# Kernel optimization log

Hardware: AMD Instinct MI355X
Metric: run time of the kernel (lower is better)

## Reference

```python
import jax, jax.numpy as jnp
import numpy as np

N_NODES = 50000
N_EDGES = 400000
IN_DIM, HID_DIM, OUT_DIM = 512, 512, 128


def sage_conv(x, src, dst, W_l, b_l, W_r, n_nodes):
    # PyG SAGEConv (mean aggr): out = lin_l(mean_{j in N(i)} x_j) + lin_r(x_i)
    msgs = x[src]                                             # [E, d_in]
    agg = jax.ops.segment_sum(msgs, dst, num_segments=n_nodes)
    deg = jax.ops.segment_sum(jnp.ones((src.shape[0],), x.dtype), dst,
                              num_segments=n_nodes)
    mean = agg / jnp.maximum(deg, 1.0)[:, None]
    return mean @ W_l + b_l + x @ W_r


def setup_inputs() -> dict:
    key = jax.random.key(0)
    ks = jax.random.split(key, 9)
    x = jax.random.normal(ks[0], (N_NODES, IN_DIM), dtype=jnp.float32)
    edge_index = jax.random.randint(ks[1], (2, N_EDGES), 0, N_NODES, dtype=jnp.int32)

    def glorot(k, d_in, d_out):
        s = (6.0 / (d_in + d_out)) ** 0.5
        return jax.random.uniform(k, (d_in, d_out), jnp.float32, -s, s)

    return {
        "x": x,
        "edge_index": edge_index,
        "W1_l": glorot(ks[2], IN_DIM, HID_DIM),
        "b1": jnp.zeros((HID_DIM,), jnp.float32),
        "W1_r": glorot(ks[3], IN_DIM, HID_DIM),
        "W2_l": glorot(ks[4], HID_DIM, HID_DIM),
        "b2": jnp.zeros((HID_DIM,), jnp.float32),
        "W2_r": glorot(ks[5], HID_DIM, HID_DIM),
        "W3_l": glorot(ks[6], HID_DIM, OUT_DIM),
        "b3": jnp.zeros((OUT_DIM,), jnp.float32),
        "W3_r": glorot(ks[7], HID_DIM, OUT_DIM),
    }


def reference(x, edge_index, W1_l, b1, W1_r, W2_l, b2, W2_r, W3_l, b3, W3_r):
    src, dst = edge_index[0], edge_index[1]
    n = x.shape[0]
    h = sage_conv(x, src, dst, W1_l, b1, W1_r, n)
    h = jax.nn.relu(h)  # dropout is identity in eval mode
    h = sage_conv(h, src, dst, W2_l, b2, W2_r, n)
    h = jax.nn.relu(h)
    h = sage_conv(h, src, dst, W3_l, b3, W3_r, n)
    return jax.nn.log_softmax(h, axis=-1)
```

## Files before the change

kernel.cpp:

```cpp
#include <hip/hip_runtime.h>
#include <hip/hip_bf16.h>


#define N_NODES 50000
#define N_EDGES 400000

typedef unsigned short u16;
typedef unsigned int u32;
typedef __attribute__((ext_vector_type(8))) short short8;
typedef __attribute__((ext_vector_type(4))) float floatx4;

#define ASYNC16(g, l)                                                      \
    __builtin_amdgcn_global_load_lds(                                      \
        (const __attribute__((address_space(1))) void*)(g),                \
        (__attribute__((address_space(3))) void*)(l), 16, 0, 0)

__device__ __forceinline__ u16 f32_to_bf16(float f) {
    u32 u = __float_as_uint(f);
    u32 r = 0x7FFFu + ((u >> 16) & 1u);
    return (u16)((u + r) >> 16);
}
__device__ __forceinline__ float bf16_to_f32(u32 lo16) {
    return __uint_as_float(lo16 << 16);
}

__global__ __launch_bounds__(256) void zero4_kernel(float4* __restrict__ p, int n4) {
    int i = blockIdx.x * 256 + threadIdx.x;
    if (i < n4) p[i] = make_float4(0.f, 0.f, 0.f, 0.f);
}

__global__ __launch_bounds__(256) void hist_kernel(const int* __restrict__ dst,
                                                   int* __restrict__ deg, int E) {
    int e = blockIdx.x * 256 + threadIdx.x;
    if (e < E) atomicAdd(&deg[dst[e]], 1);
}

__global__ __launch_bounds__(256) void scan_reduce(const int* __restrict__ v,
                                                   int* __restrict__ bsums, int n) {
    __shared__ int sh[256];
    int i = blockIdx.x * 256 + threadIdx.x;
    sh[threadIdx.x] = (i < n) ? v[i] : 0;
    __syncthreads();
    for (int off = 128; off > 0; off >>= 1) {
        if (threadIdx.x < off) sh[threadIdx.x] += sh[threadIdx.x + off];
        __syncthreads();
    }
    if (threadIdx.x == 0) bsums[blockIdx.x] = sh[0];
}

__global__ __launch_bounds__(256) void scan_sums(int* __restrict__ bsums, int nb) {
    __shared__ int sh[256];
    int t = threadIdx.x;
    int val = (t < nb) ? bsums[t] : 0;
    sh[t] = val;
    __syncthreads();
    for (int off = 1; off < 256; off <<= 1) {
        int v = (t >= off) ? sh[t - off] : 0;
        __syncthreads();
        sh[t] += v;
        __syncthreads();
    }
    if (t < nb) bsums[t] = sh[t] - val;
}

__global__ __launch_bounds__(256) void scan_final(int* __restrict__ v,
                                                  const int* __restrict__ bsums, int n) {
    __shared__ int sh[256];
    int t = threadIdx.x;
    int i = blockIdx.x * 256 + t;
    int val = (i < n) ? v[i] : 0;
    sh[t] = val;
    __syncthreads();
    for (int off = 1; off < 256; off <<= 1) {
        int x = (t >= off) ? sh[t - off] : 0;
        __syncthreads();
        sh[t] += x;
        __syncthreads();
    }
    int excl = sh[t] - val + bsums[blockIdx.x];
    if (i < n) v[i] = excl;
    if (i == n - 1) v[n] = excl + val;
}

__global__ __launch_bounds__(256) void fill_kernel(const int* __restrict__ src,
                                                   const int* __restrict__ dst,
                                                   const int* __restrict__ row_start,
                                                   int* __restrict__ cursor,
                                                   int* __restrict__ csr_src, int E) {
    int e = blockIdx.x * 256 + threadIdx.x;
    if (e < E) {
        int d = dst[e];
        int pos = row_start[d] + atomicAdd(&cursor[d], 1);
        csr_src[pos] = src[e];
    }
}

__global__ __launch_bounds__(256) void convert_bf16(const float* __restrict__ in,
                                                    u16* __restrict__ out, int n8) {
    int i = blockIdx.x * 256 + threadIdx.x;
    if (i >= n8) return;
    const float4* p = (const float4*)in + (size_t)i * 2;
    float4 v0 = p[0], v1 = p[1];
    uint4 o;
    o.x = (u32)f32_to_bf16(v0.x) | ((u32)f32_to_bf16(v0.y) << 16);
    o.y = (u32)f32_to_bf16(v0.z) | ((u32)f32_to_bf16(v0.w) << 16);
    o.z = (u32)f32_to_bf16(v1.x) | ((u32)f32_to_bf16(v1.y) << 16);
    o.w = (u32)f32_to_bf16(v1.z) | ((u32)f32_to_bf16(v1.w) << 16);
    ((uint4*)out)[i] = o;
}

__global__ __launch_bounds__(256) void transpose_w(const float* __restrict__ W,
                                                   u16* __restrict__ WT,
                                                   int K, int N) {
    __shared__ float t[32][33];
    int n0 = blockIdx.x * 32, k0 = blockIdx.y * 32;
    int c = threadIdx.x & 31, r0 = threadIdx.x >> 5;
    for (int r = r0; r < 32; r += 8)
        t[r][c] = W[(size_t)(k0 + r) * N + n0 + c];
    __syncthreads();
    for (int r = r0; r < 32; r += 8)
        WT[(size_t)(n0 + r) * K + k0 + c] = f32_to_bf16(t[c][r]);
}

__global__ __launch_bounds__(256) void gemm_bf16(
    const u16* __restrict__ A, const u16* __restrict__ BT,
    u16* __restrict__ Cl, u16* __restrict__ Cr,
    int M, int split, int nStrips, int nCols) {
    __shared__ u16 As[2][4096];
    __shared__ u16 Bs[2][4096];

    const int grp = 8 * nCols;
    int b = blockIdx.x;
    int strip = (b / grp) * 8 + (b & 7);
    int colt = (b % grp) >> 3;
    if (strip >= nStrips) return;
    const int row0 = strip * 128, col0 = colt * 128;

    const int t = threadIdx.x;
    const int w = t >> 6, lane = t & 63;
    const int wm = (w >> 1) * 64, wn = (w & 1) * 64;
    const int l15 = lane & 15, kq = lane >> 4;
    const int swz = (l15 >> 1) & 3;

    floatx4 acc[4][4];
#pragma unroll
    for (int i = 0; i < 4; ++i)
#pragma unroll
        for (int j = 0; j < 4; ++j) acc[i][j] = floatx4{0.f, 0.f, 0.f, 0.f};

    const int sr = t >> 2;
    const int sc = t & 3;
    const int swzS = (sr >> 1) & 3;
    const size_t aA0 = (size_t)min(row0 + sr, M - 1) * 512 + (sc ^ swzS) * 8;
    const size_t aA1 = (size_t)min(row0 + 64 + sr, M - 1) * 512 + (sc ^ swzS) * 8;
    const size_t aB0 = (size_t)(col0 + sr) * 512 + (sc ^ swzS) * 8;
    const size_t aB1 = (size_t)(col0 + 64 + sr) * 512 + (sc ^ swzS) * 8;
    const int d0 = w * 512;
    const int d1 = 2048 + w * 512;

    auto stage = [&](int it, int buf) {
        const int eff = it * 32;
        ASYNC16(A + aA0 + eff, &As[buf][d0]);
        ASYNC16(A + aA1 + eff, &As[buf][d1]);
        ASYNC16(BT + aB0 + eff, &Bs[buf][d0]);
        ASYNC16(BT + aB1 + eff, &Bs[buf][d1]);
    };

    stage(0, 0);
    __syncthreads();
    for (int it = 0; it < 16; ++it) {
        const int buf = it & 1;
        if (it + 1 < 16) stage(it + 1, buf ^ 1);

        const int kc = (kq ^ swz) * 8;
        short8 a[4], bfr[4];
#pragma unroll
        for (int mt = 0; mt < 4; ++mt)
            a[mt] = *(const short8*)&As[buf][(wm + mt * 16 + l15) * 32 + kc];
#pragma unroll
        for (int nt = 0; nt < 4; ++nt)
            bfr[nt] = *(const short8*)&Bs[buf][(wn + nt * 16 + l15) * 32 + kc];
#pragma unroll
        for (int mt = 0; mt < 4; ++mt)
#pragma unroll
            for (int nt = 0; nt < 4; ++nt)
                acc[mt][nt] = __builtin_amdgcn_mfma_f32_16x16x32_bf16(
                    bfr[nt], a[mt], acc[mt][nt], 0, 0, 0);
        __syncthreads();
    }

    u16* __restrict__ Cbase = (col0 < split) ? Cl : Cr;
    const int cadj = (col0 < split) ? col0 : (col0 - split);
#pragma unroll
    for (int mt = 0; mt < 4; ++mt) {
        int row = row0 + wm + mt * 16 + l15;
        if (row >= M) continue;
#pragma unroll
        for (int nt = 0; nt < 4; ++nt) {
            int c0 = cadj + wn + nt * 16 + kq * 4;
            uint2 o;
            o.x = (u32)f32_to_bf16(acc[mt][nt][0]) |
                  ((u32)f32_to_bf16(acc[mt][nt][1]) << 16);
            o.y = (u32)f32_to_bf16(acc[mt][nt][2]) |
                  ((u32)f32_to_bf16(acc[mt][nt][3]) << 16);
            *(uint2*)(Cbase + (size_t)row * split + c0) = o;
        }
    }
}

__global__ __launch_bounds__(256) void gather_add_relu512(
    const u16* __restrict__ Yl, const u16* __restrict__ Yr,
    const float* __restrict__ bias,
    const int* __restrict__ row_start, const int* __restrict__ csr_src,
    u16* __restrict__ h, int M) {
    int node = (blockIdx.x * 256 + threadIdx.x) >> 6;
    int lane = threadIdx.x & 63;
    if (node >= M) return;
    int beg = row_start[node], end = row_start[node + 1];
    float a[8] = {0.f, 0.f, 0.f, 0.f, 0.f, 0.f, 0.f, 0.f};
    for (int c = beg; c < end; c += 64) {
        int nb = min(64, end - c);
        int eid = (lane < nb) ? csr_src[c + lane] : 0;
        for (int i = 0; i < nb; ++i) {
            int s = __shfl(eid, i);
            uint4 v = ((const uint4*)(Yl + (size_t)s * 512))[lane];
            a[0] += bf16_to_f32(v.x & 0xffffu); a[1] += bf16_to_f32(v.x >> 16);
            a[2] += bf16_to_f32(v.y & 0xffffu); a[3] += bf16_to_f32(v.y >> 16);
            a[4] += bf16_to_f32(v.z & 0xffffu); a[5] += bf16_to_f32(v.z >> 16);
            a[6] += bf16_to_f32(v.w & 0xffffu); a[7] += bf16_to_f32(v.w >> 16);
        }
    }
    float inv = 1.0f / fmaxf((float)(end - beg), 1.0f);
    uint4 yr = ((const uint4*)(Yr + (size_t)node * 512))[lane];
    float4 b0 = ((const float4*)bias)[lane * 2];
    float4 b1 = ((const float4*)bias)[lane * 2 + 1];
    float v0 = fmaxf(a[0] * inv + bf16_to_f32(yr.x & 0xffffu) + b0.x, 0.f);
    float v1 = fmaxf(a[1] * inv + bf16_to_f32(yr.x >> 16)     + b0.y, 0.f);
    float v2 = fmaxf(a[2] * inv + bf16_to_f32(yr.y & 0xffffu) + b0.z, 0.f);
    float v3 = fmaxf(a[3] * inv + bf16_to_f32(yr.y >> 16)     + b0.w, 0.f);
    float v4 = fmaxf(a[4] * inv + bf16_to_f32(yr.z & 0xffffu) + b1.x, 0.f);
    float v5 = fmaxf(a[5] * inv + bf16_to_f32(yr.z >> 16)     + b1.y, 0.f);
    float v6 = fmaxf(a[6] * inv + bf16_to_f32(yr.w & 0xffffu) + b1.z, 0.f);
    float v7 = fmaxf(a[7] * inv + bf16_to_f32(yr.w >> 16)     + b1.w, 0.f);
    uint4 o;
    o.x = (u32)f32_to_bf16(v0) | ((u32)f32_to_bf16(v1) << 16);
    o.y = (u32)f32_to_bf16(v2) | ((u32)f32_to_bf16(v3) << 16);
    o.z = (u32)f32_to_bf16(v4) | ((u32)f32_to_bf16(v5) << 16);
    o.w = (u32)f32_to_bf16(v6) | ((u32)f32_to_bf16(v7) << 16);
    ((uint4*)(h + (size_t)node * 512))[lane] = o;
}

__global__ __launch_bounds__(256) void gather_add_lsm128(
    const u16* __restrict__ Yl, const u16* __restrict__ Yr,
    const float* __restrict__ bias,
    const int* __restrict__ row_start, const int* __restrict__ csr_src,
    float* __restrict__ out, int M) {
    int node = blockIdx.x * 16 + (threadIdx.x >> 4);
    int lane = threadIdx.x & 63;
    int li = lane & 15;
    int gbase = lane & 48;
    if (node >= M) return;
    int beg = row_start[node], end = row_start[node + 1];
    float a[8] = {0.f, 0.f, 0.f, 0.f, 0.f, 0.f, 0.f, 0.f};
    for (int c = beg; c < end; c += 16) {
        int nb = min(16, end - c);
        int eid = (li < nb) ? csr_src[c + li] : 0;
        for (int i = 0; i < nb; ++i) {
            int s = __shfl(eid, gbase + i);
            uint4 v = ((const uint4*)(Yl + (size_t)s * 128))[li];
            a[0] += bf16_to_f32(v.x & 0xffffu); a[1] += bf16_to_f32(v.x >> 16);
            a[2] += bf16_to_f32(v.y & 0xffffu); a[3] += bf16_to_f32(v.y >> 16);
            a[4] += bf16_to_f32(v.z & 0xffffu); a[5] += bf16_to_f32(v.z >> 16);
            a[6] += bf16_to_f32(v.w & 0xffffu); a[7] += bf16_to_f32(v.w >> 16);
        }
    }
    float inv = 1.0f / fmaxf((float)(end - beg), 1.0f);
    uint4 yr = ((const uint4*)(Yr + (size_t)node * 128))[li];
    float4 b0 = ((const float4*)bias)[li * 2];
    float4 b1 = ((const float4*)bias)[li * 2 + 1];
    float v[8];
    v[0] = a[0] * inv + bf16_to_f32(yr.x & 0xffffu) + b0.x;
    v[1] = a[1] * inv + bf16_to_f32(yr.x >> 16)     + b0.y;
    v[2] = a[2] * inv + bf16_to_f32(yr.y & 0xffffu) + b0.z;
    v[3] = a[3] * inv + bf16_to_f32(yr.y >> 16)     + b0.w;
    v[4] = a[4] * inv + bf16_to_f32(yr.z & 0xffffu) + b1.x;
    v[5] = a[5] * inv + bf16_to_f32(yr.z >> 16)     + b1.y;
    v[6] = a[6] * inv + bf16_to_f32(yr.w & 0xffffu) + b1.z;
    v[7] = a[7] * inv + bf16_to_f32(yr.w >> 16)     + b1.w;
    float m = v[0];
#pragma unroll
    for (int j = 1; j < 8; ++j) m = fmaxf(m, v[j]);
#pragma unroll
    for (int off = 1; off < 16; off <<= 1) m = fmaxf(m, __shfl_xor(m, off));
    float s = 0.f;
#pragma unroll
    for (int j = 0; j < 8; ++j) s += expf(v[j] - m);
#pragma unroll
    for (int off = 1; off < 16; off <<= 1) s += __shfl_xor(s, off);
    float ls = m + logf(s);
    float* p = out + (size_t)node * 128 + li * 8;
    *(float4*)p       = make_float4(v[0] - ls, v[1] - ls, v[2] - ls, v[3] - ls);
    *(float4*)(p + 4) = make_float4(v[4] - ls, v[5] - ls, v[6] - ls, v[7] - ls);
}

extern "C" void kernel_launch(void* const* d_in, const int* in_sizes, int n_in,
                              void* d_out, int out_size, void* d_ws, size_t ws_size,
                              hipStream_t stream) {
    const float* x    = (const float*)d_in[0];
    const int*   ei   = (const int*)d_in[1];
    const float* W1_l = (const float*)d_in[2];
    const float* b1   = (const float*)d_in[3];
    const float* W1_r = (const float*)d_in[4];
    const float* W2_l = (const float*)d_in[5];
    const float* b2   = (const float*)d_in[6];
    const float* W2_r = (const float*)d_in[7];
    const float* W3_l = (const float*)d_in[8];
    const float* b3   = (const float*)d_in[9];
    const float* W3_r = (const float*)d_in[10];
    float* out = (float*)d_out;

    const int* src = ei;
    const int* dst = ei + N_EDGES;

    char* base = (char*)d_ws;
    int* row_start = (int*)(base);
    int* cursor    = (int*)(base + 200208);
    int* bsums     = (int*)(base + 400416);
    int* csr_src   = (int*)(base + 402464);
    u16* xb  = (u16*)(base + 2002464);
    u16* h1b = (u16*)(base + 53202464);
    u16* h2b = (u16*)(base + 104402464);
    u16* Yl  = (u16*)(base + 155602464);
    u16* Yr  = (u16*)(base + 206802464);
    u16* w1T = (u16*)(base + 258002464);
    u16* w2T = (u16*)(base + 259051040);
    u16* w3T = (u16*)(base + 260099616);

    const int E = N_EDGES, M = N_NODES;
    const int nblk = (M + 255) / 256;

    zero4_kernel<<<(25154 + 255) / 256, 256, 0, stream>>>((float4*)d_ws, 25154);
    hist_kernel<<<(E + 255) / 256, 256, 0, stream>>>(dst, row_start, E);
    scan_reduce<<<nblk, 256, 0, stream>>>(row_start, bsums, M);
    scan_sums<<<1, 256, 0, stream>>>(bsums, nblk);
    scan_final<<<nblk, 256, 0, stream>>>(row_start, bsums, M);
    fill_kernel<<<(E + 255) / 256, 256, 0, stream>>>(src, dst, row_start, cursor,
                                                     csr_src, E);

    convert_bf16<<<(3200000 + 255) / 256, 256, 0, stream>>>(x, xb, 3200000);
    transpose_w<<<dim3(16, 16), 256, 0, stream>>>(W1_l, w1T, 512, 512);
    transpose_w<<<dim3(16, 16), 256, 0, stream>>>(W1_r, w1T + 512 * 512, 512, 512);
    transpose_w<<<dim3(16, 16), 256, 0, stream>>>(W2_l, w2T, 512, 512);
    transpose_w<<<dim3(16, 16), 256, 0, stream>>>(W2_r, w2T + 512 * 512, 512, 512);
    transpose_w<<<dim3(4, 16), 256, 0, stream>>>(W3_l, w3T, 512, 128);
    transpose_w<<<dim3(4, 16), 256, 0, stream>>>(W3_r, w3T + 128 * 512, 512, 128);

    const int nStrips = (M + 127) / 128;
    const int grid8 = ((nStrips + 7) / 8) * 64;
    const int grid2 = ((nStrips + 7) / 8) * 16;
    const int gblocks = (M * 64 + 255) / 256;
    const int g16blocks = (M + 15) / 16;

    gemm_bf16<<<grid8, 256, 0, stream>>>(xb, w1T, Yl, Yr, M, 512, nStrips, 8);
    gather_add_relu512<<<gblocks, 256, 0, stream>>>(Yl, Yr, b1, row_start,
                                                    csr_src, h1b, M);
    gemm_bf16<<<grid8, 256, 0, stream>>>(h1b, w2T, Yl, Yr, M, 512, nStrips, 8);
    gather_add_relu512<<<gblocks, 256, 0, stream>>>(Yl, Yr, b2, row_start,
                                                    csr_src, h2b, M);
    gemm_bf16<<<grid2, 256, 0, stream>>>(h2b, w3T, Yl, Yr, M, 128, nStrips, 2);
    gather_add_lsm128<<<g16blocks, 256, 0, stream>>>(Yl, Yr, b3, row_start,
                                                     csr_src, out, M);
}
```

Before: 656.8 us.

## Make each GEMM block loop over several column tiles with a continuous pipeline

Each GEMM workgroup now processes nCT consecutive 128-column tiles for its row strip instead of one. It runs a single double-buffered k-loop across all tiles and stores and resets the accumulators at each tile boundary. This cuts block count (4x for the 512-wide layers, 2x for the last) and keeps prefetching going across tiles, amortizing launch and prologue cost. In exchange there are fewer blocks to spread over the CUs, which may hurt occupancy and load balance, and the A tile is reloaded from global/L2 for every column tile.

After: 762.7 us. +16.1%, slower.

```diff
diff --git a/kernel.cpp b/kernel.cpp
--- a/kernel.cpp
+++ b/kernel.cpp
@@ -125,16 +125,17 @@
 __global__ __launch_bounds__(256) void gemm_bf16(
     const u16* __restrict__ A, const u16* __restrict__ BT,
     u16* __restrict__ Cl, u16* __restrict__ Cr,
-    int M, int split, int nStrips, int nCols) {
+    int M, int split, int nStrips, int nGrp, int nCT) {
     __shared__ u16 As[2][4096];
     __shared__ u16 Bs[2][4096];
 
-    const int grp = 8 * nCols;
+    const int grp = 8 * nGrp;
     int b = blockIdx.x;
     int strip = (b / grp) * 8 + (b & 7);
-    int colt = (b % grp) >> 3;
+    int ctg = (b % grp) >> 3;
     if (strip >= nStrips) return;
-    const int row0 = strip * 128, col0 = colt * 128;
+    const int row0 = strip * 128;
+    const int col0base = ctg * nCT * 128;
 
     const int t = threadIdx.x;
     const int w = t >> 6, lane = t & 63;
@@ -153,24 +154,52 @@
     const int swzS = (sr >> 1) & 3;
     const size_t aA0 = (size_t)min(row0 + sr, M - 1) * 512 + (sc ^ swzS) * 8;
     const size_t aA1 = (size_t)min(row0 + 64 + sr, M - 1) * 512 + (sc ^ swzS) * 8;
-    const size_t aB0 = (size_t)(col0 + sr) * 512 + (sc ^ swzS) * 8;
-    const size_t aB1 = (size_t)(col0 + 64 + sr) * 512 + (sc ^ swzS) * 8;
+    const size_t aB0 = (size_t)(col0base + sr) * 512 + (sc ^ swzS) * 8;
+    const size_t aB1 = (size_t)(col0base + 64 + sr) * 512 + (sc ^ swzS) * 8;
     const int d0 = w * 512;
     const int d1 = 2048 + w * 512;
 
-    auto stage = [&](int it, int buf) {
-        const int eff = it * 32;
-        ASYNC16(A + aA0 + eff, &As[buf][d0]);
-        ASYNC16(A + aA1 + eff, &As[buf][d1]);
-        ASYNC16(BT + aB0 + eff, &Bs[buf][d0]);
-        ASYNC16(BT + aB1 + eff, &Bs[buf][d1]);
+    auto stage = [&](int tt, int buf) {
+        const int it = tt & 15, ct = tt >> 4;
+        const size_t effA = (size_t)it * 32;
+        const size_t effB = (size_t)ct * 65536 + effA;
+        ASYNC16(A + aA0 + effA, &As[buf][d0]);
+        ASYNC16(A + aA1 + effA, &As[buf][d1]);
+        ASYNC16(BT + aB0 + effB, &Bs[buf][d0]);
+        ASYNC16(BT + aB1 + effB, &Bs[buf][d1]);
     };
 
+    auto storeCT = [&](int ct) {
+        const int col0 = col0base + ct * 128;
+        u16* __restrict__ Cbase = (col0 < split) ? Cl : Cr;
+        const int cadj = (col0 < split) ? col0 : (col0 - split);
+#pragma unroll
+        for (int mt = 0; mt < 4; ++mt) {
+            int row = row0 + wm + mt * 16 + l15;
+            if (row >= M) continue;
+#pragma unroll
+            for (int nt = 0; nt < 4; ++nt) {
+                int c0 = cadj + wn + nt * 16 + kq * 4;
+                uint2 o;
+                o.x = (u32)f32_to_bf16(acc[mt][nt][0]) |
+                      ((u32)f32_to_bf16(acc[mt][nt][1]) << 16);
+                o.y = (u32)f32_to_bf16(acc[mt][nt][2]) |
+                      ((u32)f32_to_bf16(acc[mt][nt][3]) << 16);
+                *(uint2*)(Cbase + (size_t)row * split + c0) = o;
+            }
+        }
+#pragma unroll
+        for (int i = 0; i < 4; ++i)
+#pragma unroll
+            for (int j = 0; j < 4; ++j) acc[i][j] = floatx4{0.f, 0.f, 0.f, 0.f};
+    };
+
+    const int nT = nCT * 16;
     stage(0, 0);
     __syncthreads();
-    for (int it = 0; it < 16; ++it) {
-        const int buf = it & 1;
-        if (it + 1 < 16) stage(it + 1, buf ^ 1);
+    for (int tt = 0; tt < nT; ++tt) {
+        const int buf = tt & 1;
+        if (tt + 1 < nT) stage(tt + 1, buf ^ 1);
 
         const int kc = (kq ^ swz) * 8;
         short8 a[4], bfr[4];
@@ -186,25 +215,10 @@
             for (int nt = 0; nt < 4; ++nt)
                 acc[mt][nt] = __builtin_amdgcn_mfma_f32_16x16x32_bf16(
                     bfr[nt], a[mt], acc[mt][nt], 0, 0, 0);
-        __syncthreads();
-    }
-
-    u16* __restrict__ Cbase = (col0 < split) ? Cl : Cr;
-    const int cadj = (col0 < split) ? col0 : (col0 - split);
-#pragma unroll
-    for (int mt = 0; mt < 4; ++mt) {
-        int row = row0 + wm + mt * 16 + l15;
-        if (row >= M) continue;
-#pragma unroll
-        for (int nt = 0; nt < 4; ++nt) {
-            int c0 = cadj + wn + nt * 16 + kq * 4;
-            uint2 o;
-            o.x = (u32)f32_to_bf16(acc[mt][nt][0]) |
-                  ((u32)f32_to_bf16(acc[mt][nt][1]) << 16);
-            o.y = (u32)f32_to_bf16(acc[mt][nt][2]) |
-                  ((u32)f32_to_bf16(acc[mt][nt][3]) << 16);
-            *(uint2*)(Cbase + (size_t)row * split + c0) = o;
-        }
+
+        if ((tt & 15) == 15) storeCT(tt >> 4);
+
+        if (tt + 1 < nT) __syncthreads();
     }
 }
 
@@ -356,18 +370,18 @@
     transpose_w<<<dim3(4, 16), 256, 0, stream>>>(W3_r, w3T + 128 * 512, 512, 128);
 
     const int nStrips = (M + 127) / 128;
-    const int grid8 = ((nStrips + 7) / 8) * 64;
-    const int grid2 = ((nStrips + 7) / 8) * 16;
+    const int grid12 = ((nStrips + 7) / 8) * 16;
+    const int grid3  = ((nStrips + 7) / 8) * 8;
     const int gblocks = (M * 64 + 255) / 256;
     const int g16blocks = (M + 15) / 16;
 
-    gemm_bf16<<<grid8, 256, 0, stream>>>(xb, w1T, Yl, Yr, M, 512, nStrips, 8);
+    gemm_bf16<<<grid12, 256, 0, stream>>>(xb, w1T, Yl, Yr, M, 512, nStrips, 2, 4);
     gather_add_relu512<<<gblocks, 256, 0, stream>>>(Yl, Yr, b1, row_start,
                                                     csr_src, h1b, M);
-    gemm_bf16<<<grid8, 256, 0, stream>>>(h1b, w2T, Yl, Yr, M, 512, nStrips, 8);
+    gemm_bf16<<<grid12, 256, 0, stream>>>(h1b, w2T, Yl, Yr, M, 512, nStrips, 2, 4);
     gather_add_relu512<<<gblocks, 256, 0, stream>>>(Yl, Yr, b2, row_start,
                                                     csr_src, h2b, M);
-    gemm_bf16<<<grid2, 256, 0, stream>>>(h2b, w3T, Yl, Yr, M, 128, nStrips, 2);
+    gemm_bf16<<<grid3, 256, 0, stream>>>(h2b, w3T, Yl, Yr, M, 128, nStrips, 1, 2);
     gather_add_lsm128<<<g16blocks, 256, 0, stream>>>(Yl, Yr, b3, row_start,
                                                      csr_src, out, M);
 }
```

## Switch GEMM to single-wave 64x64 tiles with waitcnt-based double buffering

Applied to the files above, without the earlier changes.

The bf16 GEMM moves from a 256-thread block computing a 128x128 tile to a 64-thread, single-wave block computing a 64x64 tile. The grid is resized to match. Because only one wave touches the LDS buffers, the __syncthreads barriers are replaced by explicit s_waitcnt vmcnt waits on the async global-to-LDS loads, plus a sched_barrier. This is meant to cut barrier stalls and give the scheduler more, smaller blocks, at the cost of lower data reuse per tile and more global/L2 traffic for A and B.

New measurement: 774.7 us. 1.18x slower.

```diff
diff --git a/kernel.cpp b/kernel.cpp
--- a/kernel.cpp
+++ b/kernel.cpp
@@ -122,23 +122,21 @@
         WT[(size_t)(n0 + r) * K + k0 + c] = f32_to_bf16(t[c][r]);
 }
 
-__global__ __launch_bounds__(256) void gemm_bf16(
+__global__ __launch_bounds__(64) void gemm_bf16(
     const u16* __restrict__ A, const u16* __restrict__ BT,
     u16* __restrict__ Cl, u16* __restrict__ Cr,
     int M, int split, int nStrips, int nCols) {
-    __shared__ u16 As[2][4096];
-    __shared__ u16 Bs[2][4096];
+    __shared__ u16 As[2][2048];
+    __shared__ u16 Bs[2][2048];
 
     const int grp = 8 * nCols;
     int b = blockIdx.x;
     int strip = (b / grp) * 8 + (b & 7);
     int colt = (b % grp) >> 3;
     if (strip >= nStrips) return;
-    const int row0 = strip * 128, col0 = colt * 128;
-
-    const int t = threadIdx.x;
-    const int w = t >> 6, lane = t & 63;
-    const int wm = (w >> 1) * 64, wn = (w & 1) * 64;
+    const int row0 = strip * 64, col0 = colt * 64;
+
+    const int lane = threadIdx.x;
     const int l15 = lane & 15, kq = lane >> 4;
     const int swz = (l15 >> 1) & 3;
 
@@ -148,56 +146,61 @@
 #pragma unroll
         for (int j = 0; j < 4; ++j) acc[i][j] = floatx4{0.f, 0.f, 0.f, 0.f};
 
-    const int sr = t >> 2;
-    const int sc = t & 3;
+    const int sr = lane >> 2;
+    const int sc = lane & 3;
     const int swzS = (sr >> 1) & 3;
-    const size_t aA0 = (size_t)min(row0 + sr, M - 1) * 512 + (sc ^ swzS) * 8;
-    const size_t aA1 = (size_t)min(row0 + 64 + sr, M - 1) * 512 + (sc ^ swzS) * 8;
-    const size_t aB0 = (size_t)(col0 + sr) * 512 + (sc ^ swzS) * 8;
-    const size_t aB1 = (size_t)(col0 + 64 + sr) * 512 + (sc ^ swzS) * 8;
-    const int d0 = w * 512;
-    const int d1 = 2048 + w * 512;
+    size_t aoff[4], boff[4];
+#pragma unroll
+    for (int g = 0; g < 4; ++g) {
+        aoff[g] = (size_t)min(row0 + g * 16 + sr, M - 1) * 512 + (sc ^ swzS) * 8;
+        boff[g] = (size_t)(col0 + g * 16 + sr) * 512 + (sc ^ swzS) * 8;
+    }
 
     auto stage = [&](int it, int buf) {
         const int eff = it * 32;
-        ASYNC16(A + aA0 + eff, &As[buf][d0]);
-        ASYNC16(A + aA1 + eff, &As[buf][d1]);
-        ASYNC16(BT + aB0 + eff, &Bs[buf][d0]);
-        ASYNC16(BT + aB1 + eff, &Bs[buf][d1]);
+#pragma unroll
+        for (int g = 0; g < 4; ++g) {
+            ASYNC16(A + aoff[g] + eff, &As[buf][g * 512]);
+            ASYNC16(BT + boff[g] + eff, &Bs[buf][g * 512]);
+        }
     };
 
     stage(0, 0);
-    __syncthreads();
     for (int it = 0; it < 16; ++it) {
         const int buf = it & 1;
-        if (it + 1 < 16) stage(it + 1, buf ^ 1);
+        if (it + 1 < 16) {
+            stage(it + 1, buf ^ 1);
+            asm volatile("s_waitcnt vmcnt(8)" ::: "memory");
+        } else {
+            asm volatile("s_waitcnt vmcnt(0)" ::: "memory");
+        }
+        __builtin_amdgcn_sched_barrier(0);
 
         const int kc = (kq ^ swz) * 8;
         short8 a[4], bfr[4];
 #pragma unroll
         for (int mt = 0; mt < 4; ++mt)
-            a[mt] = *(const short8*)&As[buf][(wm + mt * 16 + l15) * 32 + kc];
+            a[mt] = *(const short8*)&As[buf][(mt * 16 + l15) * 32 + kc];
 #pragma unroll
         for (int nt = 0; nt < 4; ++nt)
-            bfr[nt] = *(const short8*)&Bs[buf][(wn + nt * 16 + l15) * 32 + kc];
+            bfr[nt] = *(const short8*)&Bs[buf][(nt * 16 + l15) * 32 + kc];
 #pragma unroll
         for (int mt = 0; mt < 4; ++mt)
 #pragma unroll
             for (int nt = 0; nt < 4; ++nt)
                 acc[mt][nt] = __builtin_amdgcn_mfma_f32_16x16x32_bf16(
                     bfr[nt], a[mt], acc[mt][nt], 0, 0, 0);
-        __syncthreads();
     }
 
     u16* __restrict__ Cbase = (col0 < split) ? Cl : Cr;
     const int cadj = (col0 < split) ? col0 : (col0 - split);
 #pragma unroll
     for (int mt = 0; mt < 4; ++mt) {
-        int row = row0 + wm + mt * 16 + l15;
+        int row = row0 + mt * 16 + l15;
         if (row >= M) continue;
 #pragma unroll
         for (int nt = 0; nt < 4; ++nt) {
-            int c0 = cadj + wn + nt * 16 + kq * 4;
+            int c0 = cadj + nt * 16 + kq * 4;
             uint2 o;
             o.x = (u32)f32_to_bf16(acc[mt][nt][0]) |
                   ((u32)f32_to_bf16(acc[mt][nt][1]) << 16);
@@ -355,19 +358,19 @@
     transpose_w<<<dim3(4, 16), 256, 0, stream>>>(W3_l, w3T, 512, 128);
     transpose_w<<<dim3(4, 16), 256, 0, stream>>>(W3_r, w3T + 128 * 512, 512, 128);
 
-    const int nStrips = (M + 127) / 128;
-    const int grid8 = ((nStrips + 7) / 8) * 64;
-    const int grid2 = ((nStrips + 7) / 8) * 16;
+    const int nStrips = (M + 63) / 64;
+    const int grid12 = ((nStrips + 7) / 8) * 8 * 16;
+    const int grid3  = ((nStrips + 7) / 8) * 8 * 4;
     const int gblocks = (M * 64 + 255) / 256;
     const int g16blocks = (M + 15) / 16;
 
-    gemm_bf16<<<grid8, 256, 0, stream>>>(xb, w1T, Yl, Yr, M, 512, nStrips, 8);
+    gemm_bf16<<<grid12, 64, 0, stream>>>(xb, w1T, Yl, Yr, M, 512, nStrips, 16);
     gather_add_relu512<<<gblocks, 256, 0, stream>>>(Yl, Yr, b1, row_start,
                                                     csr_src, h1b, M);
-    gemm_bf16<<<grid8, 256, 0, stream>>>(h1b, w2T, Yl, Yr, M, 512, nStrips, 8);
+    gemm_bf16<<<grid12, 64, 0, stream>>>(h1b, w2T, Yl, Yr, M, 512, nStrips, 16);
     gather_add_relu512<<<gblocks, 256, 0, stream>>>(Yl, Yr, b2, row_start,
                                                     csr_src, h2b, M);
-    gemm_bf16<<<grid2, 256, 0, stream>>>(h2b, w3T, Yl, Yr, M, 128, nStrips, 2);
+    gemm_bf16<<<grid3, 64, 0, stream>>>(h2b, w3T, Yl, Yr, M, 128, nStrips, 4);
     gather_add_lsm128<<<g16blocks, 256, 0, stream>>>(Yl, Yr, b3, row_start,
                                                      csr_src, out, M);
 }
```

## Aggregate before transform and fuse both linears into one K=1024 GEMM

Applied to the files above, without the earlier changes.

Each layer now gathers the neighbour mean of the input features first, then runs one GEMM over the concatenated [x | mean] with stacked weights (K=1024), adding bias and ReLU in the GEMM epilogue. Before, a 2N-wide GEMM wrote separate Yl/Yr tensors, which the gather then read back. The new order removes that Yr round trip and the split output, and the final layer no longer needs the 128-wide gather. The trade-off is that the gather in layer 3 now reads 512-wide rows instead of 128-wide ones. The gather loop is also unrolled by four to keep more loads in flight.

New measurement: 727.7 us. 10.8% more time.

```diff
diff --git a/kernel.cpp b/kernel.cpp
--- a/kernel.cpp
+++ b/kernel.cpp
@@ -111,7 +111,7 @@
 
 __global__ __launch_bounds__(256) void transpose_w(const float* __restrict__ W,
                                                    u16* __restrict__ WT,
-                                                   int K, int N) {
+                                                   int K, int N, int kstride, int koff) {
     __shared__ float t[32][33];
     int n0 = blockIdx.x * 32, k0 = blockIdx.y * 32;
     int c = threadIdx.x & 31, r0 = threadIdx.x >> 5;
@@ -119,13 +119,13 @@
         t[r][c] = W[(size_t)(k0 + r) * N + n0 + c];
     __syncthreads();
     for (int r = r0; r < 32; r += 8)
-        WT[(size_t)(n0 + r) * K + k0 + c] = f32_to_bf16(t[c][r]);
-}
-
-__global__ __launch_bounds__(256) void gemm_bf16(
-    const u16* __restrict__ A, const u16* __restrict__ BT,
-    u16* __restrict__ Cl, u16* __restrict__ Cr,
-    int M, int split, int nStrips, int nCols) {
+        WT[(size_t)(n0 + r) * kstride + koff + k0 + c] = f32_to_bf16(t[c][r]);
+}
+
+__global__ __launch_bounds__(256) void gemm_bias(
+    const u16* __restrict__ A0, const u16* __restrict__ A1,
+    const u16* __restrict__ BT, const float* __restrict__ bias,
+    u16* __restrict__ C, int M, int N, int nStrips, int nCols, int relu) {
     __shared__ u16 As[2][4096];
     __shared__ u16 Bs[2][4096];
 
@@ -153,24 +153,26 @@
     const int swzS = (sr >> 1) & 3;
     const size_t aA0 = (size_t)min(row0 + sr, M - 1) * 512 + (sc ^ swzS) * 8;
     const size_t aA1 = (size_t)min(row0 + 64 + sr, M - 1) * 512 + (sc ^ swzS) * 8;
-    const size_t aB0 = (size_t)(col0 + sr) * 512 + (sc ^ swzS) * 8;
-    const size_t aB1 = (size_t)(col0 + 64 + sr) * 512 + (sc ^ swzS) * 8;
+    const size_t bB0 = (size_t)(col0 + sr) * 1024 + (sc ^ swzS) * 8;
+    const size_t bB1 = (size_t)(col0 + 64 + sr) * 1024 + (sc ^ swzS) * 8;
     const int d0 = w * 512;
     const int d1 = 2048 + w * 512;
 
     auto stage = [&](int it, int buf) {
-        const int eff = it * 32;
-        ASYNC16(A + aA0 + eff, &As[buf][d0]);
-        ASYNC16(A + aA1 + eff, &As[buf][d1]);
-        ASYNC16(BT + aB0 + eff, &Bs[buf][d0]);
-        ASYNC16(BT + aB1 + eff, &Bs[buf][d1]);
+        const u16* __restrict__ Asrc = (it < 16) ? A0 : A1;
+        const int effA = (it & 15) * 32;
+        const int effB = it * 32;
+        ASYNC16(Asrc + aA0 + effA, &As[buf][d0]);
+        ASYNC16(Asrc + aA1 + effA, &As[buf][d1]);
+        ASYNC16(BT + bB0 + effB, &Bs[buf][d0]);
+        ASYNC16(BT + bB1 + effB, &Bs[buf][d1]);
     };
 
     stage(0, 0);
     __syncthreads();
-    for (int it = 0; it < 16; ++it) {
+    for (int it = 0; it < 32; ++it) {
         const int buf = it & 1;
-        if (it + 1 < 16) stage(it + 1, buf ^ 1);
+        if (it + 1 < 32) stage(it + 1, buf ^ 1);
 
         const int kc = (kq ^ swz) * 8;
         short8 a[4], bfr[4];
@@ -189,30 +191,41 @@
         __syncthreads();
     }
 
-    u16* __restrict__ Cbase = (col0 < split) ? Cl : Cr;
-    const int cadj = (col0 < split) ? col0 : (col0 - split);
 #pragma unroll
     for (int mt = 0; mt < 4; ++mt) {
         int row = row0 + wm + mt * 16 + l15;
         if (row >= M) continue;
 #pragma unroll
         for (int nt = 0; nt < 4; ++nt) {
-            int c0 = cadj + wn + nt * 16 + kq * 4;
+            int c0 = col0 + wn + nt * 16 + kq * 4;
+            float4 bv = *(const float4*)(bias + c0);
+            float v0 = acc[mt][nt][0] + bv.x;
+            float v1 = acc[mt][nt][1] + bv.y;
+            float v2 = acc[mt][nt][2] + bv.z;
+            float v3 = acc[mt][nt][3] + bv.w;
+            if (relu) {
+                v0 = fmaxf(v0, 0.f); v1 = fmaxf(v1, 0.f);
+                v2 = fmaxf(v2, 0.f); v3 = fmaxf(v3, 0.f);
+            }
             uint2 o;
-            o.x = (u32)f32_to_bf16(acc[mt][nt][0]) |
-                  ((u32)f32_to_bf16(acc[mt][nt][1]) << 16);
-            o.y = (u32)f32_to_bf16(acc[mt][nt][2]) |
-                  ((u32)f32_to_bf16(acc[mt][nt][3]) << 16);
-            *(uint2*)(Cbase + (size_t)row * split + c0) = o;
+            o.x = (u32)f32_to_bf16(v0) | ((u32)f32_to_bf16(v1) << 16);
+            o.y = (u32)f32_to_bf16(v2) | ((u32)f32_to_bf16(v3) << 16);
+            *(uint2*)(C + (size_t)row * N + c0) = o;
         }
     }
 }
 
-__global__ __launch_bounds__(256) void gather_add_relu512(
-    const u16* __restrict__ Yl, const u16* __restrict__ Yr,
-    const float* __restrict__ bias,
+__device__ __forceinline__ void acc8(float* a, uint4 v) {
+    a[0] += bf16_to_f32(v.x & 0xffffu); a[1] += bf16_to_f32(v.x >> 16);
+    a[2] += bf16_to_f32(v.y & 0xffffu); a[3] += bf16_to_f32(v.y >> 16);
+    a[4] += bf16_to_f32(v.z & 0xffffu); a[5] += bf16_to_f32(v.z >> 16);
+    a[6] += bf16_to_f32(v.w & 0xffffu); a[7] += bf16_to_f32(v.w >> 16);
+}
+
+__global__ __launch_bounds__(256) void gather_mean512(
+    const u16* __restrict__ S,
     const int* __restrict__ row_start, const int* __restrict__ csr_src,
-    u16* __restrict__ h, int M) {
+    u16* __restrict__ mx, int M) {
     int node = (blockIdx.x * 256 + threadIdx.x) >> 6;
     int lane = threadIdx.x & 63;
     if (node >= M) return;
@@ -221,72 +234,44 @@
     for (int c = beg; c < end; c += 64) {
         int nb = min(64, end - c);
         int eid = (lane < nb) ? csr_src[c + lane] : 0;
-        for (int i = 0; i < nb; ++i) {
+        int i = 0;
+        for (; i + 4 <= nb; i += 4) {
+            int s0 = __shfl(eid, i);
+            int s1 = __shfl(eid, i + 1);
+            int s2 = __shfl(eid, i + 2);
+            int s3 = __shfl(eid, i + 3);
+            uint4 v0 = ((const uint4*)(S + (size_t)s0 * 512))[lane];
+            uint4 v1 = ((const uint4*)(S + (size_t)s1 * 512))[lane];
+            uint4 v2 = ((const uint4*)(S + (size_t)s2 * 512))[lane];
+            uint4 v3 = ((const uint4*)(S + (size_t)s3 * 512))[lane];
+            acc8(a, v0); acc8(a, v1); acc8(a, v2); acc8(a, v3);
+        }
+        for (; i < nb; ++i) {
             int s = __shfl(eid, i);
-            uint4 v = ((const uint4*)(Yl + (size_t)s * 512))[lane];
-            a[0] += bf16_to_f32(v.x & 0xffffu); a[1] += bf16_to_f32(v.x >> 16);
-            a[2] += bf16_to_f32(v.y & 0xffffu); a[3] += bf16_to_f32(v.y >> 16);
-            a[4] += bf16_to_f32(v.z & 0xffffu); a[5] += bf16_to_f32(v.z >> 16);
-            a[6] += bf16_to_f32(v.w & 0xffffu); a[7] += bf16_to_f32(v.w >> 16);
+            uint4 v = ((const uint4*)(S + (size_t)s * 512))[lane];
+            acc8(a, v);
         }
     }
     float inv = 1.0f / fmaxf((float)(end - beg), 1.0f);
-    uint4 yr = ((const uint4*)(Yr + (size_t)node * 512))[lane];
-    float4 b0 = ((const float4*)bias)[lane * 2];
-    float4 b1 = ((const float4*)bias)[lane * 2 + 1];
-    float v0 = fmaxf(a[0] * inv + bf16_to_f32(yr.x & 0xffffu) + b0.x, 0.f);
-    float v1 = fmaxf(a[1] * inv + bf16_to_f32(yr.x >> 16)     + b0.y, 0.f);
-    float v2 = fmaxf(a[2] * inv + bf16_to_f32(yr.y & 0xffffu) + b0.z, 0.f);
-    float v3 = fmaxf(a[3] * inv + bf16_to_f32(yr.y >> 16)     + b0.w, 0.f);
-    float v4 = fmaxf(a[4] * inv + bf16_to_f32(yr.z & 0xffffu) + b1.x, 0.f);
-    float v5 = fmaxf(a[5] * inv + bf16_to_f32(yr.z >> 16)     + b1.y, 0.f);
-    float v6 = fmaxf(a[6] * inv + bf16_to_f32(yr.w & 0xffffu) + b1.z, 0.f);
-    float v7 = fmaxf(a[7] * inv + bf16_to_f32(yr.w >> 16)     + b1.w, 0.f);
     uint4 o;
-    o.x = (u32)f32_to_bf16(v0) | ((u32)f32_to_bf16(v1) << 16);
-    o.y = (u32)f32_to_bf16(v2) | ((u32)f32_to_bf16(v3) << 16);
-    o.z = (u32)f32_to_bf16(v4) | ((u32)f32_to_bf16(v5) << 16);
-    o.w = (u32)f32_to_bf16(v6) | ((u32)f32_to_bf16(v7) << 16);
-    ((uint4*)(h + (size_t)node * 512))[lane] = o;
-}
-
-__global__ __launch_bounds__(256) void gather_add_lsm128(
-    const u16* __restrict__ Yl, const u16* __restrict__ Yr,
-    const float* __restrict__ bias,
-    const int* __restrict__ row_start, const int* __restrict__ csr_src,
-    float* __restrict__ out, int M) {
+    o.x = (u32)f32_to_bf16(a[0] * inv) | ((u32)f32_to_bf16(a[1] * inv) << 16);
+    o.y = (u32)f32_to_bf16(a[2] * inv) | ((u32)f32_to_bf16(a[3] * inv) << 16);
+    o.z = (u32)f32_to_bf16(a[4] * inv) | ((u32)f32_to_bf16(a[5] * inv) << 16);
+    o.w = (u32)f32_to_bf16(a[6] * inv) | ((u32)f32_to_bf16(a[7] * inv) << 16);
+    ((uint4*)(mx + (size_t)node * 512))[lane] = o;
+}
+
+__global__ __launch_bounds__(256) void lsm_dense128(
+    const u16* __restrict__ Y, float* __restrict__ out, int M) {
     int node = blockIdx.x * 16 + (threadIdx.x >> 4);
-    int lane = threadIdx.x & 63;
-    int li = lane & 15;
-    int gbase = lane & 48;
+    int li = threadIdx.x & 15;
     if (node >= M) return;
-    int beg = row_start[node], end = row_start[node + 1];
-    float a[8] = {0.f, 0.f, 0.f, 0.f, 0.f, 0.f, 0.f, 0.f};
-    for (int c = beg; c < end; c += 16) {
-        int nb = min(16, end - c);
-        int eid = (li < nb) ? csr_src[c + li] : 0;
-        for (int i = 0; i < nb; ++i) {
-            int s = __shfl(eid, gbase + i);
-            uint4 v = ((const uint4*)(Yl + (size_t)s * 128))[li];
-            a[0] += bf16_to_f32(v.x & 0xffffu); a[1] += bf16_to_f32(v.x >> 16);
-            a[2] += bf16_to_f32(v.y & 0xffffu); a[3] += bf16_to_f32(v.y >> 16);
-            a[4] += bf16_to_f32(v.z & 0xffffu); a[5] += bf16_to_f32(v.z >> 16);
-            a[6] += bf16_to_f32(v.w & 0xffffu); a[7] += bf16_to_f32(v.w >> 16);
-        }
-    }
-    float inv = 1.0f / fmaxf((float)(end - beg), 1.0f);
-    uint4 yr = ((const uint4*)(Yr + (size_t)node * 128))[li];
-    float4 b0 = ((const float4*)bias)[li * 2];
-    float4 b1 = ((const float4*)bias)[li * 2 + 1];
+    uint4 yv = ((const uint4*)(Y + (size_t)node * 128))[li];
     float v[8];
-    v[0] = a[0] * inv + bf16_to_f32(yr.x & 0xffffu) + b0.x;
-    v[1] = a[1] * inv + bf16_to_f32(yr.x >> 16)     + b0.y;
-    v[2] = a[2] * inv + bf16_to_f32(yr.y & 0xffffu) + b0.z;
-    v[3] = a[3] * inv + bf16_to_f32(yr.y >> 16)     + b0.w;
-    v[4] = a[4] * inv + bf16_to_f32(yr.z & 0xffffu) + b1.x;
-    v[5] = a[5] * inv + bf16_to_f32(yr.z >> 16)     + b1.y;
-    v[6] = a[6] * inv + bf16_to_f32(yr.w & 0xffffu) + b1.z;
-    v[7] = a[7] * inv + bf16_to_f32(yr.w >> 16)     + b1.w;
+    v[0] = bf16_to_f32(yv.x & 0xffffu); v[1] = bf16_to_f32(yv.x >> 16);
+    v[2] = bf16_to_f32(yv.y & 0xffffu); v[3] = bf16_to_f32(yv.y >> 16);
+    v[4] = bf16_to_f32(yv.z & 0xffffu); v[5] = bf16_to_f32(yv.z >> 16);
+    v[6] = bf16_to_f32(yv.w & 0xffffu); v[7] = bf16_to_f32(yv.w >> 16);
     float m = v[0];
 #pragma unroll
     for (int j = 1; j < 8; ++j) m = fmaxf(m, v[j]);
@@ -330,11 +315,11 @@
     u16* xb  = (u16*)(base + 2002464);
     u16* h1b = (u16*)(base + 53202464);
     u16* h2b = (u16*)(base + 104402464);
-    u16* Yl  = (u16*)(base + 155602464);
-    u16* Yr  = (u16*)(base + 206802464);
-    u16* w1T = (u16*)(base + 258002464);
-    u16* w2T = (u16*)(base + 259051040);
-    u16* w3T = (u16*)(base + 260099616);
+    u16* mx  = (u16*)(base + 155602464);
+    u16* y3  = (u16*)(base + 206802464);
+    u16* w1T = (u16*)(base + 219602464);
+    u16* w2T = (u16*)(base + 220651040);
+    u16* w3T = (u16*)(base + 221699616);
 
     const int E = N_EDGES, M = N_NODES;
     const int nblk = (M + 255) / 256;
@@ -348,26 +333,27 @@
                                                      csr_src, E);
 
     convert_bf16<<<(3200000 + 255) / 256, 256, 0, stream>>>(x, xb, 3200000);
-    transpose_w<<<dim3(16, 16), 256, 0, stream>>>(W1_l, w1T, 512, 512);
-    transpose_w<<<dim3(16, 16), 256, 0, stream>>>(W1_r, w1T + 512 * 512, 512, 512);
-    transpose_w<<<dim3(16, 16), 256, 0, stream>>>(W2_l, w2T, 512, 512);
-    transpose_w<<<dim3(16, 16), 256, 0, stream>>>(W2_r, w2T + 512 * 512, 512, 512);
-    transpose_w<<<dim3(4, 16), 256, 0, stream>>>(W3_l, w3T, 512, 128);
-    transpose_w<<<dim3(4, 16), 256, 0, stream>>>(W3_r, w3T + 128 * 512, 512, 128);
+    transpose_w<<<dim3(16, 16), 256, 0, stream>>>(W1_r, w1T, 512, 512, 1024, 0);
+    transpose_w<<<dim3(16, 16), 256, 0, stream>>>(W1_l, w1T, 512, 512, 1024, 512);
+    transpose_w<<<dim3(16, 16), 256, 0, stream>>>(W2_r, w2T, 512, 512, 1024, 0);
+    transpose_w<<<dim3(16, 16), 256, 0, stream>>>(W2_l, w2T, 512, 512, 1024, 512);
+    transpose_w<<<dim3(4, 16), 256, 0, stream>>>(W3_r, w3T, 512, 128, 1024, 0);
+    transpose_w<<<dim3(4, 16), 256, 0, stream>>>(W3_l, w3T, 512, 128, 1024, 512);
 
     const int nStrips = (M + 127) / 128;
-    const int grid8 = ((nStrips + 7) / 8) * 64;
-    const int grid2 = ((nStrips + 7) / 8) * 16;
+    const int gridN512 = ((nStrips + 7) / 8) * 8 * 4;
+    const int gridN128 = ((nStrips + 7) / 8) * 8 * 1;
     const int gblocks = (M * 64 + 255) / 256;
     const int g16blocks = (M + 15) / 16;
 
-    gemm_bf16<<<grid8, 256, 0, stream>>>(xb, w1T, Yl, Yr, M, 512, nStrips, 8);
-    gather_add_relu512<<<gblocks, 256, 0, stream>>>(Yl, Yr, b1, row_start,
-                                                    csr_src, h1b, M);
-    gemm_bf16<<<grid8, 256, 0, stream>>>(h1b, w2T, Yl, Yr, M, 512, nStrips, 8);
-    gather_add_relu512<<<gblocks, 256, 0, stream>>>(Yl, Yr, b2, row_start,
-                                                    csr_src, h2b, M);
-    gemm_bf16<<<grid2, 256, 0, stream>>>(h2b, w3T, Yl, Yr, M, 128, nStrips, 2);
-    gather_add_lsm128<<<g16blocks, 256, 0, stream>>>(Yl, Yr, b3, row_start,
-                                                     csr_src, out, M);
-}
+    gather_mean512<<<gblocks, 256, 0, stream>>>(xb, row_start, csr_src, mx, M);
+    gemm_bias<<<gridN512, 256, 0, stream>>>(xb, mx, w1T, b1, h1b, M, 512,
+                                            nStrips, 4, 1);
+    gather_mean512<<<gblocks, 256, 0, stream>>>(h1b, row_start, csr_src, mx, M);
+    gemm_bias<<<gridN512, 256, 0, stream>>>(h1b, mx, w2T, b2, h2b, M, 512,
+                                            nStrips, 4, 1);
+    gather_mean512<<<gblocks, 256, 0, stream>>>(h2b, row_start, csr_src, mx, M);
+    gemm_bias<<<gridN128, 256, 0, stream>>>(h2b, mx, w3T, b3, y3, M, 128,
+                                            nStrips, 1, 0);
+    lsm_dense128<<<g16blocks, 256, 0, stream>>>(y3, out, M);
+}
```
